# Optimization experiments

Measured on AMD Instinct MI355X. Metric: run time of the kernel, lower is better.

## Reference

```python
import jax, jax.numpy as jnp
import numpy as np

B, S, HID = 2, 2048, 2048
NH, HD, G = 16, 128, 4
NKV = NH // G  # 4
ROPE_THETA = 10000.0


def _xavier(key, shape):
    fan_in, fan_out = shape
    lim = float(np.sqrt(6.0 / (fan_in + fan_out)))
    return jax.random.uniform(key, shape, jnp.float32, -lim, lim)


def setup_inputs() -> dict:
    key = jax.random.key(0)
    ks = jax.random.split(key, 6)
    hidden_states = jax.random.normal(ks[0], (B, S, HID), jnp.float32)
    # mask==True means MASKED (code adds mask * -1e9): causal upper triangle
    causal = jnp.triu(jnp.ones((S, S), jnp.bool_), k=1)
    mask = jnp.broadcast_to(causal[None, None], (B, 1, S, S))
    return {
        "hidden_states": hidden_states,
        "mask": mask,
        "Wq": _xavier(ks[1], (HID, NH * HD)),
        "bq": jnp.zeros((NH * HD,), jnp.float32),
        "Wk": _xavier(ks[2], (HID, NKV * HD)),
        "bk": jnp.zeros((NKV * HD,), jnp.float32),
        "Wv": _xavier(ks[3], (HID, NKV * HD)),
        "bv": jnp.zeros((NKV * HD,), jnp.float32),
        "Wo": _xavier(ks[4], (NH * HD, HID)),
        "bo": jnp.zeros((HID,), jnp.float32),
    }


def _rope_cos_sin(seq_len, head_dim, dtype):
    half = head_dim // 2
    inv_freq = 1.0 / (ROPE_THETA ** (jnp.arange(0, half, dtype=jnp.float32) / half))
    ang = jnp.arange(seq_len, dtype=jnp.float32)[:, None] * inv_freq[None, :]  # [S, half]
    # shape [1, S, 1, half] for broadcasting over (B, S, H, half)
    return jnp.cos(ang)[None, :, None, :].astype(dtype), jnp.sin(ang)[None, :, None, :].astype(dtype)


def _apply_rope(x, cos, sin):
    half = x.shape[-1] // 2
    x1, x2 = x[..., :half], x[..., half:]
    return jnp.concatenate([x1 * cos - x2 * sin, x1 * sin + x2 * cos], axis=-1)


def reference(hidden_states, mask, Wq, bq, Wk, bk, Wv, bv, Wo, bo):
    b, s, _ = hidden_states.shape
    scale = 1.0 / jnp.sqrt(jnp.asarray(HD, hidden_states.dtype))

    q = (hidden_states @ Wq + bq).reshape(b, s, NH, HD)
    k = (hidden_states @ Wk + bk).reshape(b, s, NKV, HD)
    v = (hidden_states @ Wv + bv).reshape(b, s, NKV, HD)

    cos, sin = _rope_cos_sin(s, HD, hidden_states.dtype)
    q = _apply_rope(q, cos, sin)
    k = _apply_rope(k, cos, sin)

    q = jnp.transpose(q, (0, 2, 1, 3))          # [B, NH, S, D]
    k = jnp.transpose(k, (0, 2, 1, 3))          # [B, NKV, S, D]
    v = jnp.transpose(v, (0, 2, 1, 3))          # [B, NKV, S, D]

    # GQA: group query heads instead of repeating K/V (same math as jnp.repeat)
    qg = q.reshape(b, NKV, G, s, HD)
    scores = jnp.einsum('bngqd,bnkd->bngqk', qg, k) * scale  # [B, NKV, G, S, S]

    maskf = mask.astype(scores.dtype)[:, :, None]  # [B, 1, 1, S, S]
    scores = scores + maskf * (-1e9)

    probs = jax.nn.softmax(scores, axis=-1)
    out = jnp.einsum('bngqk,bnkd->bngqd', probs, v)          # [B, NKV, G, S, D]
    out = out.reshape(b, NH, s, HD).transpose(0, 2, 1, 3).reshape(b, s, NH * HD)
    return out @ Wo + bo
```

## Files before the change

kernel.cpp:

```cpp
#include <hip/hip_runtime.h>
#include <hip/hip_bf16.h>

#define B_ 2
#define S_ 2048
#define HID_ 2048
#define NH_ 16
#define HD_ 128
#define NKV_ 4
#define M_ (B_*S_)
#define NQKV_ 3072
#define QSCALE2 0.12752464484148957f
#define DEFER_THR 11.5425f
#define NSPLIT 4

typedef __bf16 bf16x8 __attribute__((ext_vector_type(8)));
typedef float f32x4 __attribute__((ext_vector_type(4)));
typedef float f32x16 __attribute__((ext_vector_type(16)));

typedef __attribute__((address_space(1))) const unsigned int gas_uint;
typedef __attribute__((address_space(3))) unsigned int las_uint;

__device__ __forceinline__ unsigned short f2bfu(float x) {
  __hip_bfloat16 h = __float2bfloat16(x);
  return __builtin_bit_cast(unsigned short, h);
}

__device__ __forceinline__ unsigned int pack2bf(float lo, float hi) {
  return (unsigned int)f2bfu(lo) | ((unsigned int)f2bfu(hi) << 16);
}

__device__ __forceinline__ float bflo(unsigned int u) {
  return __builtin_bit_cast(float, u << 16);
}
__device__ __forceinline__ float bfhi(unsigned int u) {
  return __builtin_bit_cast(float, u & 0xffff0000u);
}

__device__ __forceinline__ void gload_lds16(const void* g, void* l) {
  __builtin_amdgcn_global_load_lds((gas_uint*)g, (las_uint*)l, 16, 0, 0);
}


__global__ void k_cvt(const float* __restrict__ src, unsigned short* __restrict__ dst, int n4) {
  int i = blockIdx.x * 256 + threadIdx.x;
  if (i >= n4) return;
  float4 v = ((const float4*)src)[i];
  ushort4 o;
  o.x = f2bfu(v.x); o.y = f2bfu(v.y); o.z = f2bfu(v.z); o.w = f2bfu(v.w);
  ((ushort4*)dst)[i] = o;
}

__global__ void k_tcvt(const float* __restrict__ src, unsigned short* __restrict__ dst, int R, int C) {
  __shared__ float t[32][33];
  int bc = blockIdx.x * 32, br = blockIdx.y * 32;
  int tx = threadIdx.x & 31, ty = threadIdx.x >> 5;
  for (int i = ty; i < 32; i += 8)
    t[i][tx] = src[(size_t)(br + i) * C + bc + tx];
  __syncthreads();
  for (int i = ty; i < 32; i += 8)
    dst[(size_t)(bc + i) * R + br + tx] = f2bfu(t[tx][i]);
}

__global__ void k_bias(const float* __restrict__ bq, const float* __restrict__ bk,
                       const float* __restrict__ bv, float* __restrict__ out) {
  int i = blockIdx.x * 256 + threadIdx.x;
  float v = (i < 2048) ? bq[i] : (i < 2560 ? bk[i - 2048] : bv[i - 2560]);
  out[i] = v;
}

__global__ void k_ropetab(float* __restrict__ cosT, float* __restrict__ sinT) {
  int idx = blockIdx.x * 256 + threadIdx.x;
  int s = idx >> 6, i = idx & 63;
  float invf = expf(-(float)i * (9.210340371976184f / 64.f));
  float ang = (float)s * invf;
  cosT[idx] = cosf(ang);
  sinT[idx] = sinf(ang);
}

__global__ void k_ropeq(const float* __restrict__ Cq, const float* __restrict__ cosT,
                        const float* __restrict__ sinT, unsigned short* __restrict__ Qr) {
  int idx = blockIdx.x * 256 + threadIdx.x;
  int i = idx & 63, h = (idx >> 6) & (NH_ - 1), m = idx >> 10;
  int s = m & (S_ - 1), b = m >> 11;
  const float* row = Cq + (size_t)m * NQKV_ + h * HD_;
  float x1 = row[i], x2 = row[i + 64];
  float c = cosT[(s << 6) + i], sn = sinT[(s << 6) + i];
  size_t base = ((size_t)(b * NH_ + h) * S_ + s) * HD_;
  Qr[base + i]      = f2bfu((x1 * c - x2 * sn) * QSCALE2);
  Qr[base + i + 64] = f2bfu((x1 * sn + x2 * c) * QSCALE2);
}

__global__ void k_ropek(const float* __restrict__ Cq, const float* __restrict__ cosT,
                        const float* __restrict__ sinT, unsigned short* __restrict__ Kr) {
  int idx = blockIdx.x * 256 + threadIdx.x;
  int i = idx & 63, kv = (idx >> 6) & (NKV_ - 1), m = idx >> 8;
  int s = m & (S_ - 1), b = m >> 11;
  const float* row = Cq + (size_t)m * NQKV_ + 2048 + kv * HD_;
  float x1 = row[i], x2 = row[i + 64];
  float c = cosT[(s << 6) + i], sn = sinT[(s << 6) + i];
  size_t base = ((size_t)(b * NKV_ + kv) * S_ + s) * HD_;
  Kr[base + i]      = f2bfu(x1 * c - x2 * sn);
  Kr[base + i + 64] = f2bfu(x1 * sn + x2 * c);
}

__global__ void k_vt(const float* __restrict__ Cq, unsigned short* __restrict__ Vt) {
  __shared__ float t[32][129];
  int bx = blockIdx.x;
  int st = bx & 63, kv = (bx >> 6) & 3, b = bx >> 8;
  int s0 = st * 32;
  int tid = threadIdx.x;
  for (int j = 0; j < 16; ++j) {
    int idx = j * 256 + tid;
    int si = idx >> 7, d = idx & 127;
    t[si][d] = Cq[(size_t)(b * S_ + s0 + si) * NQKV_ + 2560 + kv * HD_ + d];
  }
  __syncthreads();
  for (int j = 0; j < 16; ++j) {
    int idx = j * 256 + tid;
    int d = idx >> 5, si = idx & 31;
    Vt[((size_t)(b * NKV_ + kv) * HD_ + d) * S_ + s0 + si] = f2bfu(t[si][d]);
  }
}


__global__ __launch_bounds__(256, 2)
void k_gemm(const unsigned short* __restrict__ A, const unsigned short* __restrict__ Bt,
            const float* __restrict__ bias, float* __restrict__ C,
            int Md, int Nd, int Kd) {
  __shared__ __align__(16) unsigned short As[128 * 64];
  __shared__ __align__(16) unsigned short Bs[128 * 64];
  int nt = Nd >> 7;
  int nwg = (Md >> 7) * nt;
  int bid = blockIdx.x;
  int wg = bid;
  if ((nwg & 7) == 0) { int cpx = nwg >> 3; wg = (bid & 7) * cpx + (bid >> 3); }
  int bm = wg / nt, bn = wg - bm * nt;
  int tid = threadIdx.x;
  int lane = tid & 63, w = tid >> 6;
  int wm = (w >> 1) << 6, wn = (w & 1) << 6;
  int lr = lane & 15, lg = lane >> 4;
  f32x4 acc[4][4] = {};

  const int chunkbase = w << 2;
  const int boff = lane << 4;
  const int nK = Kd >> 6;
  const size_t rowstride = (size_t)Kd * 2;

  for (int kt = 0; kt < nK; ++kt) {
#pragma unroll
    for (int i = 0; i < 4; ++i) {
      int off = ((chunkbase + i) << 10) + boff;
      int row = off >> 7;
      int colb = off & 127;
      int scolb = colb ^ ((row & 7) << 4);
      const char* ga = (const char*)A + (size_t)(bm * 128 + row) * rowstride + (kt << 7) + scolb;
      const char* gb = (const char*)Bt + (size_t)(bn * 128 + row) * rowstride + (kt << 7) + scolb;
      gload_lds16(ga, (char*)As + ((chunkbase + i) << 10));
      gload_lds16(gb, (char*)Bs + ((chunkbase + i) << 10));
    }
    __syncthreads();
#pragma unroll
    for (int kk = 0; kk < 2; ++kk) {
      bf16x8 a[4], b[4];
      int kb = ((kk << 5) + (lg << 3)) << 1;
#pragma unroll
      for (int mi = 0; mi < 4; ++mi) {
        int row = wm + (mi << 4) + lr;
        a[mi] = *(const bf16x8*)((const char*)As + (row << 7) + (kb ^ ((row & 7) << 4)));
      }
#pragma unroll
      for (int ni = 0; ni < 4; ++ni) {
        int row = wn + (ni << 4) + lr;
        b[ni] = *(const bf16x8*)((const char*)Bs + (row << 7) + (kb ^ ((row & 7) << 4)));
      }
#pragma unroll
      for (int mi = 0; mi < 4; ++mi)
#pragma unroll
        for (int ni = 0; ni < 4; ++ni)
          acc[mi][ni] = __builtin_amdgcn_mfma_f32_16x16x32_bf16(a[mi], b[ni], acc[mi][ni], 0, 0, 0);
    }
    __syncthreads();
  }
#pragma unroll
  for (int mi = 0; mi < 4; ++mi) {
    int r0 = bm * 128 + wm + (mi << 4) + (lg << 2);
#pragma unroll
    for (int ni = 0; ni < 4; ++ni) {
      int col = bn * 128 + wn + (ni << 4) + lr;
      float bz = bias[col];
#pragma unroll
      for (int r = 0; r < 4; ++r)
        C[(size_t)(r0 + r) * Nd + col] = acc[mi][ni][r] + bz;
    }
  }
}


__global__ __launch_bounds__(256, 2)
void k_attn(const unsigned short* __restrict__ Qr, const unsigned short* __restrict__ Kr,
            const unsigned short* __restrict__ Vt,
            unsigned short* __restrict__ Po0, unsigned short* __restrict__ Po1,
            unsigned short* __restrict__ Po2, unsigned short* __restrict__ Po3,
            float2* __restrict__ Ml) {
  __shared__ __align__(16) unsigned short Ks[2][64 * 128];
  int bid = blockIdx.x;
  int g = bid & 7;
  int b = g >> 2, kvh = g & 3;
  int r = bid >> 3;
  int split = r & 3;
  int r2 = r >> 2;
  int hg = r2 >> 4;
  int qt = 15 - (r2 & 15);
  int h = (kvh << 2) + hg;
  int tid = threadIdx.x, lane = tid & 63, w = tid >> 6;
  int ql = lane & 31, hi = lane >> 5;
  int q0 = (qt << 7) + (w << 5);
  int qrow = q0 + ql;

  const unsigned short* Qp = Qr + (((size_t)(b * NH_ + h) * S_) << 7);
  const unsigned short* Kp = Kr + (((size_t)(b * NKV_ + kvh) * S_) << 7);
  const unsigned short* Vp = Vt + (((size_t)(b * NKV_ + kvh) * HD_) << 11);

  bf16x8 qa[8];
#pragma unroll
  for (int c = 0; c < 8; ++c)
    qa[c] = *(const bf16x8*)(Qp + (((size_t)qrow) << 7) + (c << 4) + (hi << 3));

  f32x16 acc[4] = {};
  float m_r = -1e30f, l_r = 0.f;

  const int T = (qt + 1) << 1;
  const int nit = (T - split + 3) >> 2;

#define STAGE_K(bsel, t)                                                        \
  {                                                                             \
    const char* kbase = (const char*)Kp + ((size_t)(t) << 14);                  \
    _Pragma("unroll")                                                           \
    for (int i_ = 0; i_ < 4; ++i_) {                                            \
      int woff_ = (i_ << 12) + (w << 10);                                       \
      int off_ = woff_ + (lane << 4);                                           \
      int row_ = off_ >> 8;                                                     \
      int colb_ = off_ & 255;                                                   \
      int scolb_ = colb_ ^ ((row_ & 15) << 4);                                  \
      gload_lds16(kbase + ((size_t)row_ << 8) + scolb_,                         \
                  (char*)Ks[bsel] + woff_);                                     \
    }                                                                           \
  }

  STAGE_K(0, split);
  __syncthreads();

  for (int i = 0; i < nit; ++i) {
    int t = split + (i << 2);
    if (i + 1 < nit) STAGE_K((i + 1) & 1, t + 4);
    const char* Kb = (const char*)Ks[i & 1];

#pragma unroll
    for (int sub = 0; sub < 2; ++sub) {
      int kvbase = (t << 6) + (sub << 5);
      if (kvbase > q0 + 31) continue;

      f32x16 st = {};
      int krow = (sub << 5) + ql;
      int sw = (krow & 15) << 4;
#pragma unroll
      for (int c = 0; c < 8; ++c) {
        int cb = (c << 5) + (hi << 4);
        bf16x8 kf = *(const bf16x8*)(Kb + (krow << 8) + (cb ^ sw));
        st = __builtin_amdgcn_mfma_f32_32x32x16_bf16(kf, qa[c], st, 0, 0, 0);
      }
      if (kvbase + 31 > q0) {
#pragma unroll
        for (int rr = 0; rr < 16; ++rr) {
          int kv = kvbase + (rr & 3) + ((rr >> 2) << 3) + (hi << 2);
          if (kv > qrow) st[rr] = -1e30f;
        }
      }
      float pmax = st[0];
#pragma unroll
      for (int rr = 1; rr < 16; ++rr) pmax = fmaxf(pmax, st[rr]);
      pmax = fmaxf(pmax, __shfl_xor(pmax, 32));
      if (!__all(pmax <= m_r + DEFER_THR)) {
        float mn = fmaxf(m_r, pmax);
        float al = exp2f(m_r - mn);
        m_r = mn;
        l_r *= al;
#pragma unroll
        for (int dc = 0; dc < 4; ++dc) acc[dc] = acc[dc] * al;
      }
      float p[16];
      float ps = 0.f;
#pragma unroll
      for (int rr = 0; rr < 16; ++rr) { p[rr] = exp2f(st[rr] - m_r); ps += p[rr]; }
      ps += __shfl_xor(ps, 32);
      l_r += ps;
      unsigned int W[8];
#pragma unroll
      for (int i2 = 0; i2 < 8; ++i2) W[i2] = pack2bf(p[2 * i2], p[2 * i2 + 1]);
      unsigned int pw0 = __shfl_xor(W[0], 32), pw1 = __shfl_xor(W[1], 32);
      unsigned int pw2 = __shfl_xor(W[2], 32), pw3 = __shfl_xor(W[3], 32);
      unsigned int pw4 = __shfl_xor(W[4], 32), pw5 = __shfl_xor(W[5], 32);
      unsigned int pw6 = __shfl_xor(W[6], 32), pw7 = __shfl_xor(W[7], 32);
      uint4 u0, u1;
      u0.x = hi ? pw2 : W[0];
      u0.y = hi ? pw3 : W[1];
      u0.z = hi ? W[2] : pw0;
      u0.w = hi ? W[3] : pw1;
      u1.x = hi ? pw6 : W[4];
      u1.y = hi ? pw7 : W[5];
      u1.z = hi ? W[6] : pw4;
      u1.w = hi ? W[7] : pw5;
      bf16x8 pa0 = __builtin_bit_cast(bf16x8, u0);
      bf16x8 pa1 = __builtin_bit_cast(bf16x8, u1);
#pragma unroll
      for (int dc = 0; dc < 4; ++dc) {
        const unsigned short* vrow = Vp + (((size_t)((dc << 5) + ql)) << 11) + kvbase + (hi << 3);
        bf16x8 vf0 = *(const bf16x8*)(vrow);
        bf16x8 vf1 = *(const bf16x8*)(vrow + 16);
        acc[dc] = __builtin_amdgcn_mfma_f32_32x32x16_bf16(vf0, pa0, acc[dc], 0, 0, 0);
        acc[dc] = __builtin_amdgcn_mfma_f32_32x32x16_bf16(vf1, pa1, acc[dc], 0, 0, 0);
      }
    }
    __syncthreads();
  }

  unsigned short* Pob = (split == 0) ? Po0 : (split == 1) ? Po1 : (split == 2) ? Po2 : Po3;
  float inv = (l_r > 0.f) ? (1.f / l_r) : 0.f;
  unsigned short* obase = Pob + ((((size_t)(b * S_) + qrow)) << 11) + (h << 7) + (hi << 2);
#pragma unroll
  for (int dc = 0; dc < 4; ++dc)
#pragma unroll
    for (int gq = 0; gq < 4; ++gq) {
      ushort4 o;
      o.x = f2bfu(acc[dc][4 * gq + 0] * inv);
      o.y = f2bfu(acc[dc][4 * gq + 1] * inv);
      o.z = f2bfu(acc[dc][4 * gq + 2] * inv);
      o.w = f2bfu(acc[dc][4 * gq + 3] * inv);
      *(ushort4*)(obase + (dc << 5) + (gq << 3)) = o;
    }
  if (hi == 0)
    Ml[(size_t)split * (M_ * NH_) + ((size_t)(b * S_) + qrow) * NH_ + h] = make_float2(m_r, l_r);
}

__global__ void k_comb(const unsigned short* __restrict__ Po0, const unsigned short* __restrict__ Po1,
                       const unsigned short* __restrict__ Po2, const unsigned short* __restrict__ Po3,
                       const float2* __restrict__ Ml, unsigned short* __restrict__ Ob) {
  int idx = blockIdx.x * 256 + threadIdx.x;
  int c = idx >> 4;
  float2 a0 = Ml[c], a1 = Ml[c + M_ * NH_], a2 = Ml[c + 2 * M_ * NH_], a3 = Ml[c + 3 * M_ * NH_];
  float m = fmaxf(fmaxf(a0.x, a1.x), fmaxf(a2.x, a3.x));
  float w0 = a0.y * exp2f(a0.x - m);
  float w1 = a1.y * exp2f(a1.x - m);
  float w2 = a2.y * exp2f(a2.x - m);
  float w3 = a3.y * exp2f(a3.x - m);
  float inv = 1.f / (w0 + w1 + w2 + w3);
  w0 *= inv; w1 *= inv; w2 *= inv; w3 *= inv;
  size_t e = (size_t)idx << 3;
  uint4 v0 = *(const uint4*)(Po0 + e);
  uint4 v1 = *(const uint4*)(Po1 + e);
  uint4 v2 = *(const uint4*)(Po2 + e);
  uint4 v3 = *(const uint4*)(Po3 + e);
  uint4 o;
  o.x = pack2bf(w0 * bflo(v0.x) + w1 * bflo(v1.x) + w2 * bflo(v2.x) + w3 * bflo(v3.x),
                w0 * bfhi(v0.x) + w1 * bfhi(v1.x) + w2 * bfhi(v2.x) + w3 * bfhi(v3.x));
  o.y = pack2bf(w0 * bflo(v0.y) + w1 * bflo(v1.y) + w2 * bflo(v2.y) + w3 * bflo(v3.y),
                w0 * bfhi(v0.y) + w1 * bfhi(v1.y) + w2 * bfhi(v2.y) + w3 * bfhi(v3.y));
  o.z = pack2bf(w0 * bflo(v0.z) + w1 * bflo(v1.z) + w2 * bflo(v2.z) + w3 * bflo(v3.z),
                w0 * bfhi(v0.z) + w1 * bfhi(v1.z) + w2 * bfhi(v2.z) + w3 * bfhi(v3.z));
  o.w = pack2bf(w0 * bflo(v0.w) + w1 * bflo(v1.w) + w2 * bflo(v2.w) + w3 * bflo(v3.w),
                w0 * bfhi(v0.w) + w1 * bfhi(v1.w) + w2 * bfhi(v2.w) + w3 * bfhi(v3.w));
  *(uint4*)(Ob + e) = o;
}


extern "C" void kernel_launch(void* const* d_in, const int* in_sizes, int n_in,
                              void* d_out, int out_size, void* d_ws, size_t ws_size,
                              hipStream_t stream) {
  const float* X  = (const float*)d_in[0];
  const float* Wq = (const float*)d_in[2];
  const float* bq = (const float*)d_in[3];
  const float* Wk = (const float*)d_in[4];
  const float* bk = (const float*)d_in[5];
  const float* Wv = (const float*)d_in[6];
  const float* bv = (const float*)d_in[7];
  const float* Wo = (const float*)d_in[8];
  const float* bo = (const float*)d_in[9];
  float* out = (float*)d_out;

  char* ws = (char*)d_ws;
  unsigned short* Xb  = (unsigned short*)(ws);
  unsigned short* Wt  = (unsigned short*)(ws + 16777216);
  unsigned short* Wot = (unsigned short*)(ws + 29360128);
  float* Bqkv         = (float*)(ws + 37748736);
  float* cosT         = (float*)(ws + 37761024);
  float* sinT         = (float*)(ws + 38285312);
  float* Cqkv         = (float*)(ws + 38809600);
  unsigned short* Qr  = (unsigned short*)(ws + 89141248);
  unsigned short* Kr  = (unsigned short*)(ws + 105918464);
  unsigned short* Vtb = (unsigned short*)(ws + 110112768);
  unsigned short* Ob  = (unsigned short*)(ws + 114307072);
  unsigned short* Po0 = (unsigned short*)(ws);
  unsigned short* Po1 = (unsigned short*)(ws + 38809600);
  unsigned short* Po2 = (unsigned short*)(ws + 38809600 + 16777216);
  unsigned short* Po3 = (unsigned short*)(ws + 38809600 + 33554432);
  float2* Ml          = (float2*)(ws + 16777216);

  k_cvt<<<(M_ * HID_ / 4 + 255) / 256, 256, 0, stream>>>(X, Xb, M_ * HID_ / 4);
  k_tcvt<<<dim3(2048 / 32, 2048 / 32), 256, 0, stream>>>(Wq, Wt, 2048, 2048);
  k_tcvt<<<dim3(512 / 32, 2048 / 32), 256, 0, stream>>>(Wk, Wt + 2048 * 2048, 2048, 512);
  k_tcvt<<<dim3(512 / 32, 2048 / 32), 256, 0, stream>>>(Wv, Wt + 2560 * 2048, 2048, 512);
  k_tcvt<<<dim3(2048 / 32, 2048 / 32), 256, 0, stream>>>(Wo, Wot, 2048, 2048);
  k_bias<<<12, 256, 0, stream>>>(bq, bk, bv, Bqkv);
  k_ropetab<<<S_ * 64 / 256, 256, 0, stream>>>(cosT, sinT);

  k_gemm<<<(M_ / 128) * (NQKV_ / 128), 256, 0, stream>>>(Xb, Wt, Bqkv, Cqkv, M_, NQKV_, HID_);

  k_ropeq<<<M_ * NH_ * 64 / 256, 256, 0, stream>>>(Cqkv, cosT, sinT, Qr);
  k_ropek<<<M_ * NKV_ * 64 / 256, 256, 0, stream>>>(Cqkv, cosT, sinT, Kr);
  k_vt<<<B_ * NKV_ * (S_ / 32), 256, 0, stream>>>(Cqkv, Vtb);

  k_attn<<<B_ * NH_ * (S_ / 128) * NSPLIT, 256, 0, stream>>>(Qr, Kr, Vtb, Po0, Po1, Po2, Po3, Ml);
  k_comb<<<M_ * HID_ / 8 / 256, 256, 0, stream>>>(Po0, Po1, Po2, Po3, Ml, Ob);

  k_gemm<<<(M_ / 128) * (HID_ / 128), 256, 0, stream>>>(Ob, Wot, bo, out, M_, HID_, NH_ * HD_);
}
```

Baseline: 255.2 us.

## Store QKV projection in bf16 and prefetch V fragments earlier in attention

The QKV GEMM now writes its output as bf16 instead of fp32. The rope and V-transpose kernels read this halved intermediate, which cuts global memory traffic. The attention kernel issues its V-fragment loads right after the QK MFMAs so their latency overlaps the softmax. It also halves the cross-lane shuffles by exchanging only the needed P words and deferring the row-sum reduction to the end. The cost is an extra bf16 rounding of Q/K/V before RoPE, and V now held in registers during softmax, which raises register pressure.

```diff
diff --git a/kernel.cpp b/kernel.cpp
--- a/kernel.cpp
+++ b/kernel.cpp
@@ -35,6 +35,9 @@
 __device__ __forceinline__ float bfhi(unsigned int u) {
   return __builtin_bit_cast(float, u & 0xffff0000u);
 }
+__device__ __forceinline__ float bf2f(unsigned short u) {
+  return __builtin_bit_cast(float, (unsigned int)u << 16);
+}
 
 __device__ __forceinline__ void gload_lds16(const void* g, void* l) {
   __builtin_amdgcn_global_load_lds((gas_uint*)g, (las_uint*)l, 16, 0, 0);
@@ -77,34 +80,34 @@
   sinT[idx] = sinf(ang);
 }
 
-__global__ void k_ropeq(const float* __restrict__ Cq, const float* __restrict__ cosT,
+__global__ void k_ropeq(const unsigned short* __restrict__ Cq, const float* __restrict__ cosT,
                         const float* __restrict__ sinT, unsigned short* __restrict__ Qr) {
   int idx = blockIdx.x * 256 + threadIdx.x;
   int i = idx & 63, h = (idx >> 6) & (NH_ - 1), m = idx >> 10;
   int s = m & (S_ - 1), b = m >> 11;
-  const float* row = Cq + (size_t)m * NQKV_ + h * HD_;
-  float x1 = row[i], x2 = row[i + 64];
+  const unsigned short* row = Cq + (size_t)m * NQKV_ + h * HD_;
+  float x1 = bf2f(row[i]), x2 = bf2f(row[i + 64]);
   float c = cosT[(s << 6) + i], sn = sinT[(s << 6) + i];
   size_t base = ((size_t)(b * NH_ + h) * S_ + s) * HD_;
   Qr[base + i]      = f2bfu((x1 * c - x2 * sn) * QSCALE2);
   Qr[base + i + 64] = f2bfu((x1 * sn + x2 * c) * QSCALE2);
 }
 
-__global__ void k_ropek(const float* __restrict__ Cq, const float* __restrict__ cosT,
+__global__ void k_ropek(const unsigned short* __restrict__ Cq, const float* __restrict__ cosT,
                         const float* __restrict__ sinT, unsigned short* __restrict__ Kr) {
   int idx = blockIdx.x * 256 + threadIdx.x;
   int i = idx & 63, kv = (idx >> 6) & (NKV_ - 1), m = idx >> 8;
   int s = m & (S_ - 1), b = m >> 11;
-  const float* row = Cq + (size_t)m * NQKV_ + 2048 + kv * HD_;
-  float x1 = row[i], x2 = row[i + 64];
+  const unsigned short* row = Cq + (size_t)m * NQKV_ + 2048 + kv * HD_;
+  float x1 = bf2f(row[i]), x2 = bf2f(row[i + 64]);
   float c = cosT[(s << 6) + i], sn = sinT[(s << 6) + i];
   size_t base = ((size_t)(b * NKV_ + kv) * S_ + s) * HD_;
   Kr[base + i]      = f2bfu(x1 * c - x2 * sn);
   Kr[base + i + 64] = f2bfu(x1 * sn + x2 * c);
 }
 
-__global__ void k_vt(const float* __restrict__ Cq, unsigned short* __restrict__ Vt) {
-  __shared__ float t[32][129];
+__global__ void k_vt(const unsigned short* __restrict__ Cq, unsigned short* __restrict__ Vt) {
+  __shared__ unsigned short t[32][136];
   int bx = blockIdx.x;
   int st = bx & 63, kv = (bx >> 6) & 3, b = bx >> 8;
   int s0 = st * 32;
@@ -118,14 +121,15 @@
   for (int j = 0; j < 16; ++j) {
     int idx = j * 256 + tid;
     int d = idx >> 5, si = idx & 31;
-    Vt[((size_t)(b * NKV_ + kv) * HD_ + d) * S_ + s0 + si] = f2bfu(t[si][d]);
-  }
-}
-
-
+    Vt[((size_t)(b * NKV_ + kv) * HD_ + d) * S_ + s0 + si] = t[si][d];
+  }
+}
+
+
+template <bool BF16OUT>
 __global__ __launch_bounds__(256, 2)
 void k_gemm(const unsigned short* __restrict__ A, const unsigned short* __restrict__ Bt,
-            const float* __restrict__ bias, float* __restrict__ C,
+            const float* __restrict__ bias, void* __restrict__ Cv,
             int Md, int Nd, int Kd) {
   __shared__ __align__(16) unsigned short As[128 * 64];
   __shared__ __align__(16) unsigned short Bs[128 * 64];
@@ -189,8 +193,13 @@
       int col = bn * 128 + wn + (ni << 4) + lr;
       float bz = bias[col];
 #pragma unroll
-      for (int r = 0; r < 4; ++r)
-        C[(size_t)(r0 + r) * Nd + col] = acc[mi][ni][r] + bz;
+      for (int r = 0; r < 4; ++r) {
+        float v = acc[mi][ni][r] + bz;
+        if constexpr (BF16OUT)
+          ((unsigned short*)Cv)[(size_t)(r0 + r) * Nd + col] = f2bfu(v);
+        else
+          ((float*)Cv)[(size_t)(r0 + r) * Nd + col] = v;
+      }
     }
   }
 }
@@ -269,6 +278,13 @@
         bf16x8 kf = *(const bf16x8*)(Kb + (krow << 8) + (cb ^ sw));
         st = __builtin_amdgcn_mfma_f32_32x32x16_bf16(kf, qa[c], st, 0, 0, 0);
       }
+      bf16x8 vf[8];
+#pragma unroll
+      for (int dc = 0; dc < 4; ++dc) {
+        const unsigned short* vrow = Vp + (((size_t)((dc << 5) + ql)) << 11) + kvbase + (hi << 3);
+        vf[2 * dc]     = *(const bf16x8*)(vrow);
+        vf[2 * dc + 1] = *(const bf16x8*)(vrow + 16);
+      }
       if (kvbase + 31 > q0) {
 #pragma unroll
         for (int rr = 0; rr < 16; ++rr) {
@@ -292,40 +308,37 @@
       float ps = 0.f;
 #pragma unroll
       for (int rr = 0; rr < 16; ++rr) { p[rr] = exp2f(st[rr] - m_r); ps += p[rr]; }
-      ps += __shfl_xor(ps, 32);
       l_r += ps;
       unsigned int W[8];
 #pragma unroll
       for (int i2 = 0; i2 < 8; ++i2) W[i2] = pack2bf(p[2 * i2], p[2 * i2 + 1]);
-      unsigned int pw0 = __shfl_xor(W[0], 32), pw1 = __shfl_xor(W[1], 32);
-      unsigned int pw2 = __shfl_xor(W[2], 32), pw3 = __shfl_xor(W[3], 32);
-      unsigned int pw4 = __shfl_xor(W[4], 32), pw5 = __shfl_xor(W[5], 32);
-      unsigned int pw6 = __shfl_xor(W[6], 32), pw7 = __shfl_xor(W[7], 32);
+      unsigned int r0 = __shfl_xor(hi ? W[0] : W[2], 32);
+      unsigned int r1 = __shfl_xor(hi ? W[1] : W[3], 32);
+      unsigned int r2v = __shfl_xor(hi ? W[4] : W[6], 32);
+      unsigned int r3 = __shfl_xor(hi ? W[5] : W[7], 32);
       uint4 u0, u1;
-      u0.x = hi ? pw2 : W[0];
-      u0.y = hi ? pw3 : W[1];
-      u0.z = hi ? W[2] : pw0;
-      u0.w = hi ? W[3] : pw1;
-      u1.x = hi ? pw6 : W[4];
-      u1.y = hi ? pw7 : W[5];
-      u1.z = hi ? W[6] : pw4;
-      u1.w = hi ? W[7] : pw5;
+      u0.x = hi ? r0 : W[0];
+      u0.y = hi ? r1 : W[1];
+      u0.z = hi ? W[2] : r0;
+      u0.w = hi ? W[3] : r1;
+      u1.x = hi ? r2v : W[4];
+      u1.y = hi ? r3 : W[5];
+      u1.z = hi ? W[6] : r2v;
+      u1.w = hi ? W[7] : r3;
       bf16x8 pa0 = __builtin_bit_cast(bf16x8, u0);
       bf16x8 pa1 = __builtin_bit_cast(bf16x8, u1);
 #pragma unroll
       for (int dc = 0; dc < 4; ++dc) {
-        const unsigned short* vrow = Vp + (((size_t)((dc << 5) + ql)) << 11) + kvbase + (hi << 3);
-        bf16x8 vf0 = *(const bf16x8*)(vrow);
-        bf16x8 vf1 = *(const bf16x8*)(vrow + 16);
-        acc[dc] = __builtin_amdgcn_mfma_f32_32x32x16_bf16(vf0, pa0, acc[dc], 0, 0, 0);
-        acc[dc] = __builtin_amdgcn_mfma_f32_32x32x16_bf16(vf1, pa1, acc[dc], 0, 0, 0);
+        acc[dc] = __builtin_amdgcn_mfma_f32_32x32x16_bf16(vf[2 * dc], pa0, acc[dc], 0, 0, 0);
+        acc[dc] = __builtin_amdgcn_mfma_f32_32x32x16_bf16(vf[2 * dc + 1], pa1, acc[dc], 0, 0, 0);
       }
     }
     __syncthreads();
   }
 
+  float l_tot = l_r + __shfl_xor(l_r, 32);
   unsigned short* Pob = (split == 0) ? Po0 : (split == 1) ? Po1 : (split == 2) ? Po2 : Po3;
-  float inv = (l_r > 0.f) ? (1.f / l_r) : 0.f;
+  float inv = (l_tot > 0.f) ? (1.f / l_tot) : 0.f;
   unsigned short* obase = Pob + ((((size_t)(b * S_) + qrow)) << 11) + (h << 7) + (hi << 2);
 #pragma unroll
   for (int dc = 0; dc < 4; ++dc)
@@ -339,7 +352,7 @@
       *(ushort4*)(obase + (dc << 5) + (gq << 3)) = o;
     }
   if (hi == 0)
-    Ml[(size_t)split * (M_ * NH_) + ((size_t)(b * S_) + qrow) * NH_ + h] = make_float2(m_r, l_r);
+    Ml[(size_t)split * (M_ * NH_) + ((size_t)(b * S_) + qrow) * NH_ + h] = make_float2(m_r, l_tot);
 }
 
 __global__ void k_comb(const unsigned short* __restrict__ Po0, const unsigned short* __restrict__ Po1,
@@ -394,7 +407,7 @@
   float* Bqkv         = (float*)(ws + 37748736);
   float* cosT         = (float*)(ws + 37761024);
   float* sinT         = (float*)(ws + 38285312);
-  float* Cqkv         = (float*)(ws + 38809600);
+  unsigned short* Cqkvb = (unsigned short*)(ws + 38809600);
   unsigned short* Qr  = (unsigned short*)(ws + 89141248);
   unsigned short* Kr  = (unsigned short*)(ws + 105918464);
   unsigned short* Vtb = (unsigned short*)(ws + 110112768);
@@ -413,14 +426,14 @@
   k_bias<<<12, 256, 0, stream>>>(bq, bk, bv, Bqkv);
   k_ropetab<<<S_ * 64 / 256, 256, 0, stream>>>(cosT, sinT);
 
-  k_gemm<<<(M_ / 128) * (NQKV_ / 128), 256, 0, stream>>>(Xb, Wt, Bqkv, Cqkv, M_, NQKV_, HID_);
-
-  k_ropeq<<<M_ * NH_ * 64 / 256, 256, 0, stream>>>(Cqkv, cosT, sinT, Qr);
-  k_ropek<<<M_ * NKV_ * 64 / 256, 256, 0, stream>>>(Cqkv, cosT, sinT, Kr);
-  k_vt<<<B_ * NKV_ * (S_ / 32), 256, 0, stream>>>(Cqkv, Vtb);
+  k_gemm<true><<<(M_ / 128) * (NQKV_ / 128), 256, 0, stream>>>(Xb, Wt, Bqkv, Cqkvb, M_, NQKV_, HID_);
+
+  k_ropeq<<<M_ * NH_ * 64 / 256, 256, 0, stream>>>(Cqkvb, cosT, sinT, Qr);
+  k_ropek<<<M_ * NKV_ * 64 / 256, 256, 0, stream>>>(Cqkvb, cosT, sinT, Kr);
+  k_vt<<<B_ * NKV_ * (S_ / 32), 256, 0, stream>>>(Cqkvb, Vtb);
 
   k_attn<<<B_ * NH_ * (S_ / 128) * NSPLIT, 256, 0, stream>>>(Qr, Kr, Vtb, Po0, Po1, Po2, Po3, Ml);
   k_comb<<<M_ * HID_ / 8 / 256, 256, 0, stream>>>(Po0, Po1, Po2, Po3, Ml, Ob);
 
-  k_gemm<<<(M_ / 128) * (HID_ / 128), 256, 0, stream>>>(Ob, Wot, bo, out, M_, HID_, NH_ * HD_);
-}
+  k_gemm<false><<<(M_ / 128) * (HID_ / 128), 256, 0, stream>>>(Ob, Wot, bo, out, M_, HID_, NH_ * HD_);
+}
```

Result: faster. 248.8 us (-2.5%).
